# Optimization experiments

Measured on AMD Instinct MI355X. Metric: run time of the kernel, lower is better.

Reference implementation:

```python
import jax, jax.numpy as jnp
import numpy as np

MARGIN = 2.0   # self.m
SCALE = 30.0   # cosine-head logit scale


def setup_inputs() -> dict:
    key = jax.random.key(0)
    k1, k2, k3 = jax.random.split(key, 3)
    B, D, C = 8192, 256, 5994
    emb = jax.random.normal(k1, (B, D), dtype=jnp.float32)
    W = jax.random.normal(k2, (C, D), dtype=jnp.float32) * 0.05
    y = jax.random.randint(k3, (B,), 0, C, dtype=jnp.int32)
    # first half domain 0 (main), second half domain 1 (target)
    y_d = jnp.concatenate([jnp.zeros(B // 2, jnp.int32), jnp.ones(B // 2, jnp.int32)])
    return {"emb": emb, "W": W, "y": y, "y_d": y_d}


def _clf_head(emb, W, y):
    # cosine-similarity classifier + cross-entropy (standard ASV clf head)
    e = emb / (jnp.linalg.norm(emb, axis=1, keepdims=True) + 1e-12)
    w = W / (jnp.linalg.norm(W, axis=1, keepdims=True) + 1e-12)
    logits = SCALE * (e @ w.T)                     # [B, C]
    logp = jax.nn.log_softmax(logits, axis=-1)
    loss = -jnp.mean(jnp.take_along_axis(logp, y[:, None], axis=1))
    acc = jnp.mean((jnp.argmax(logits, axis=-1) == y).astype(jnp.float32))
    return loss, acc


def reference(emb, W, y, y_d):
    B, D = emb.shape
    H = B // 2
    idx = jnp.arange(B)
    # faithful scatter: domain-0 rows -> main_emb[i]; domain-1 rows -> target_emb[i % H]
    # out-of-range sentinel H is dropped (rows with wrong domain stay zero)
    main_idx = jnp.where(y_d == 0, idx, H)
    tgt_idx = jnp.where(y_d != 0, idx % H, H)
    main_emb = jnp.zeros((H, D), emb.dtype).at[main_idx].set(emb, mode="drop")
    target_emb = jnp.zeros((H, D), emb.dtype).at[tgt_idx].set(emb, mode="drop")

    loss_c, acc = _clf_head(emb, W, y)

    # pairwise diffs: even rows main[i]-main[(i+1)%H] (label 1), odd rows main[i]-target[i] (label 0)
    pos_diff = main_emb - jnp.roll(main_emb, -1, axis=0)  # [H, D]
    neg_diff = main_emb - target_emb                      # [H, D]
    das_diff = jnp.stack([pos_diff, neg_diff], axis=1).reshape(B, D)
    das_label = jnp.tile(jnp.array([1.0, 0.0], emb.dtype), H)  # [B]

    das_dist = jnp.linalg.norm(das_diff, axis=1)
    das_loss = jnp.mean((1.0 - das_label) * das_dist ** 2
                        + das_label * jnp.maximum(MARGIN - das_dist, 0.0) ** 2)
    das_dist_mean = jnp.mean(jax.lax.stop_gradient(das_dist))
    return (loss_c, das_loss, acc, das_dist_mean)
```

## Files before the change

### kernel.cpp

```cpp
#include <hip/hip_runtime.h>
#include <hip/hip_bf16.h>

#define B_ROWS 8192
#define DIM 256
#define C_CLS 5994
#define N_CHUNK 188
#define NSPL 16
#define H_HALF 4096
#define SCALE_F 30.0f
#define MAXL 30.0f
#define EXPC 43.2808512266689f

#if defined(__has_builtin)
#if __has_builtin(__builtin_amdgcn_exp2f)
#define EXP2(x) __builtin_amdgcn_exp2f(x)
#endif
#endif
#ifndef EXP2
#define EXP2(x) exp2f(x)
#endif

typedef float f32x16 __attribute__((ext_vector_type(16)));
typedef long long ll;
typedef ll ll2 __attribute__((ext_vector_type(2)));

__global__ __launch_bounds__(256)
void k_pack(const float* __restrict__ emb, const float* __restrict__ W,
            char* __restrict__ en_blk, char* __restrict__ wn_blk,
            float* __restrict__ rne, float* __restrict__ rnw,
            float* __restrict__ accum) {
  __shared__ float ssm[256];
  __shared__ float rnl[32];
  const int b = blockIdx.x;
  const int t = threadIdx.x;
  if (b == 0 && t < 8) accum[t] = 0.f;
  const bool isW = b >= (B_ROWS/32);
  const int tile = isW ? b - (B_ROWS/32) : b;
  const int l31 = t & 31;
  const int row = tile*32 + l31;
  const float* __restrict__ src = isW ? W : emb;
  const bool rv = (!isW) || (row < C_CLS);

  float v[4][8];
  float ss = 0.f;
  #pragma unroll
  for (int i=0;i<4;i++) {
    const int d0 = ((t>>6) + i*4)*16 + ((t>>5)&1)*8;
    if (rv) {
      float4 x0 = *(const float4*)(src + (size_t)row*DIM + d0);
      float4 x1 = *(const float4*)(src + (size_t)row*DIM + d0 + 4);
      v[i][0]=x0.x; v[i][1]=x0.y; v[i][2]=x0.z; v[i][3]=x0.w;
      v[i][4]=x1.x; v[i][5]=x1.y; v[i][6]=x1.z; v[i][7]=x1.w;
      ss += x0.x*x0.x + x0.y*x0.y + x0.z*x0.z + x0.w*x0.w
          + x1.x*x1.x + x1.y*x1.y + x1.z*x1.z + x1.w*x1.w;
    } else {
      #pragma unroll
      for (int j=0;j<8;j++) v[i][j] = 0.f;
    }
  }
  ssm[t] = ss;
  __syncthreads();
  if (t < 32) {
    float s = 0.f;
    #pragma unroll
    for (int j=0;j<8;j++) s += ssm[t + j*32];
    float rn = 1.0f/(sqrtf(s) + 1e-12f);
    rnl[t] = rn;
    int rw = tile*32 + t;
    if (!isW) rne[rw] = rn;
    else if (rw < C_CLS) rnw[rw] = rn;
  }
  __syncthreads();
  const float rn = rnl[l31];
  char* __restrict__ dst = (isW ? wn_blk : en_blk) + (size_t)tile*8192;
  const int kbase = (t>>5)*512 + l31*16;
  (void)kbase;
  #pragma unroll
  for (int i=0;i<4;i++) {
    const int kk = (t>>6) + i*4;
    const int off = (kk>>1)*1024 + ((t>>5)&1)*512 + l31*16 + (kk&1)*8;
    int d0 = 0, d1 = 0;
    d0 = __builtin_amdgcn_cvt_pk_fp8_f32(v[i][0]*rn, v[i][1]*rn, d0, false);
    d0 = __builtin_amdgcn_cvt_pk_fp8_f32(v[i][2]*rn, v[i][3]*rn, d0, true);
    d1 = __builtin_amdgcn_cvt_pk_fp8_f32(v[i][4]*rn, v[i][5]*rn, d1, false);
    d1 = __builtin_amdgcn_cvt_pk_fp8_f32(v[i][6]*rn, v[i][7]*rn, d1, true);
    uint2 u; u.x = (unsigned)d0; u.y = (unsigned)d1;
    *(uint2*)(dst + off) = u;
  }
}

__global__ __launch_bounds__(256, 2)
void k_logits(const char* __restrict__ en_blk, const char* __restrict__ wn_blk,
              float* __restrict__ psum, unsigned* __restrict__ pkey) {
  const int split = blockIdx.x & (NSPL-1);
  const int panel = blockIdx.x / NSPL;
  const int wid  = threadIdx.x >> 6;
  const int lane = threadIdx.x & 63;
  const int l31  = lane & 31;
  const int lh   = lane >> 5;
  const int tile = panel*4 + wid;
  (void)lh;

  ll2 a[8];
  const char* ab = en_blk + (size_t)tile*8192 + lane*16;
  #pragma unroll
  for (int j=0;j<8;j++) a[j] = *(const ll2*)(ab + j*1024);

  float ssum[16]; unsigned key[16];
  #pragma unroll
  for (int r=0;r<16;r++){ ssum[r]=0.f; key[r]=0u; }

  const int nit = (N_CHUNK - split + NSPL - 1) / NSPL;
  const char* p = wn_blk + (size_t)split*8192 + lane*16;
  const ptrdiff_t STEP = (ptrdiff_t)NSPL*8192;

  ll2 b0[4], b1[4];
  #pragma unroll
  for (int j=0;j<4;j++) b0[j] = *(const ll2*)(p + j*1024);
  #pragma unroll
  for (int j=0;j<4;j++) b1[j] = *(const ll2*)(p + (j+4)*1024);

  unsigned colu = (unsigned)(split*32 + l31);
  for (int it = 0; it < nit-1; ++it) {
    const char* pn = p + STEP;
    f32x16 acc = {};
    #pragma unroll
    for (int j=0;j<4;j++) {
      acc = __builtin_amdgcn_mfma_f32_32x32x16_fp8_fp8(a[j][0], b0[j][0], acc, 0,0,0);
      acc = __builtin_amdgcn_mfma_f32_32x32x16_fp8_fp8(a[j][1], b0[j][1], acc, 0,0,0);
    }
    #pragma unroll
    for (int j=0;j<4;j++) b0[j] = *(const ll2*)(pn + j*1024);
    #pragma unroll
    for (int j=0;j<4;j++) {
      acc = __builtin_amdgcn_mfma_f32_32x32x16_fp8_fp8(a[j+4][0], b1[j][0], acc, 0,0,0);
      acc = __builtin_amdgcn_mfma_f32_32x32x16_fp8_fp8(a[j+4][1], b1[j][1], acc, 0,0,0);
    }
    #pragma unroll
    for (int j=0;j<4;j++) b1[j] = *(const ll2*)(pn + (j+4)*1024);
    #pragma unroll
    for (int r=0;r<16;r++) {
      float x = acc[r];
      ssum[r] += EXP2(fmaf(x, EXPC, -EXPC));
      unsigned ky = (__float_as_uint(x + 2.0f) & 0xFFFFE000u) | colu;
      key[r] = ky > key[r] ? ky : key[r];
    }
    colu += NSPL*32;
    p = pn;
  }
  {
    f32x16 acc = {};
    #pragma unroll
    for (int j=0;j<4;j++) {
      acc = __builtin_amdgcn_mfma_f32_32x32x16_fp8_fp8(a[j][0], b0[j][0], acc, 0,0,0);
      acc = __builtin_amdgcn_mfma_f32_32x32x16_fp8_fp8(a[j][1], b0[j][1], acc, 0,0,0);
    }
    #pragma unroll
    for (int j=0;j<4;j++) {
      acc = __builtin_amdgcn_mfma_f32_32x32x16_fp8_fp8(a[j+4][0], b1[j][0], acc, 0,0,0);
      acc = __builtin_amdgcn_mfma_f32_32x32x16_fp8_fp8(a[j+4][1], b1[j][1], acc, 0,0,0);
    }
    #pragma unroll
    for (int r=0;r<16;r++) {
      float x = acc[r];
      ssum[r] += EXP2(fmaf(x, EXPC, -EXPC));
      unsigned ky = (__float_as_uint(x + 2.0f) & 0xFFFFE000u) | colu;
      key[r] = ky > key[r] ? ky : key[r];
    }
  }

  #pragma unroll
  for (int off=1; off<32; off<<=1) {
    #pragma unroll
    for (int r=0;r<16;r++) {
      ssum[r] += __shfl_xor(ssum[r], off);
      unsigned o = __shfl_xor(key[r], off);
      key[r] = o > key[r] ? o : key[r];
    }
  }
  if (l31 == 0) {
    const int rowbase = tile*32;
    #pragma unroll
    for (int r=0;r<16;r++) {
      int row = rowbase + (r&3) + 8*(r>>2) + 4*(lane>>5);
      psum[split*B_ROWS + row] = ssum[r];
      pkey[split*B_ROWS + row] = key[r];
    }
  }
}

__global__ __launch_bounds__(256)
void k_tail(const float* __restrict__ emb, const float* __restrict__ W,
            const int* __restrict__ y, const int* __restrict__ y_d,
            const float* __restrict__ rne, const float* __restrict__ rnw,
            const float* __restrict__ psum, const unsigned* __restrict__ pkey,
            float* __restrict__ accum, float* __restrict__ out) {
  __shared__ float s0[4], s1[4];
  const int wid = threadIdx.x >> 6, lane = threadIdx.x & 63;
  if (blockIdx.x < 128) {
    float lacc = 0.f, cacc = 0.f;
    for (int row = blockIdx.x*4 + wid; row < B_ROWS; row += 512) {
      const int yc = y[row];
      float4 e = *(const float4*)(emb + (size_t)row*DIM + lane*4);
      float4 w = *(const float4*)(W + (size_t)yc*DIM + lane*4);
      float d = e.x*w.x + e.y*w.y + e.z*w.z + e.w*w.w;
      #pragma unroll
      for (int off=1; off<64; off<<=1) d += __shfl_xor(d, off);
      float S = 0.f; unsigned km = 0u;
      if (lane < NSPL) {
        S = psum[lane*B_ROWS + row];
        km = pkey[lane*B_ROWS + row];
      }
      #pragma unroll
      for (int off=1; off<NSPL; off<<=1) {
        S += __shfl_xor(S, off);
        unsigned o = __shfl_xor(km, off);
        if (o > km) km = o;
      }
      if (lane == 0) {
        float ly = SCALE_F * d * rne[row] * rnw[yc];
        lacc += MAXL + logf(S) - ly;
        cacc += ((km & 0x1FFFu) == (unsigned)yc) ? 1.f : 0.f;
      }
    }
    if (lane == 0) { s0[wid] = lacc; s1[wid] = cacc; }
    __syncthreads();
    if (threadIdx.x == 0) {
      atomicAdd(&accum[0], s0[0]+s0[1]+s0[2]+s0[3]);
      atomicAdd(&accum[1], s1[0]+s1[1]+s1[2]+s1[3]);
    }
  } else {
    float a2 = 0.f, a3 = 0.f;
    for (int i = (blockIdx.x-128)*4 + wid; i < H_HALF; i += 256) {
      const int j = (i+1) & (H_HALF-1);
      const int di = y_d[i], dj = y_d[j], dih = y_d[i + H_HALF];
      float4 z = {0.f,0.f,0.f,0.f};
      float4 mi = (di==0)  ? *(const float4*)(emb + (size_t)i*DIM + lane*4) : z;
      float4 mj = (dj==0)  ? *(const float4*)(emb + (size_t)j*DIM + lane*4) : z;
      float4 ti = (dih!=0) ? *(const float4*)(emb + (size_t)(i+H_HALF)*DIM + lane*4)
                           : ((di!=0) ? *(const float4*)(emb + (size_t)i*DIM + lane*4) : z);
      float px = mi.x-mj.x, py = mi.y-mj.y, pz = mi.z-mj.z, pw = mi.w-mj.w;
      float nx = mi.x-ti.x, ny = mi.y-ti.y, nz = mi.z-ti.z, nw = mi.w-ti.w;
      float sp = px*px+py*py+pz*pz+pw*pw;
      float sn = nx*nx+ny*ny+nz*nz+nw*nw;
      #pragma unroll
      for (int off=1; off<64; off<<=1) { sp += __shfl_xor(sp, off); sn += __shfl_xor(sn, off); }
      if (lane == 0) {
        float dp = sqrtf(sp), dn = sqrtf(sn);
        float m = fmaxf(2.0f - dp, 0.f);
        a2 += m*m + dn*dn;
        a3 += dp + dn;
      }
    }
    if (lane == 0) { s0[wid] = a2; s1[wid] = a3; }
    __syncthreads();
    if (threadIdx.x == 0) {
      atomicAdd(&accum[2], s0[0]+s0[1]+s0[2]+s0[3]);
      atomicAdd(&accum[3], s1[0]+s1[1]+s1[2]+s1[3]);
    }
  }
  if (threadIdx.x == 0) {
    __threadfence();
    unsigned* cnt = (unsigned*)(accum + 4);
    unsigned done = atomicAdd(cnt, 1u);
    if (done == 191u) {
      float v0 = atomicAdd(&accum[0], 0.f);
      float v1 = atomicAdd(&accum[1], 0.f);
      float v2 = atomicAdd(&accum[2], 0.f);
      float v3 = atomicAdd(&accum[3], 0.f);
      out[0] = v0 * (1.0f/B_ROWS);
      out[1] = v2 * (1.0f/B_ROWS);
      out[2] = v1 * (1.0f/B_ROWS);
      out[3] = v3 * (1.0f/B_ROWS);
    }
  }
}

extern "C" void kernel_launch(void* const* d_in, const int* in_sizes, int n_in,
                              void* d_out, int out_size, void* d_ws, size_t ws_size,
                              hipStream_t stream) {
  const float* emb = (const float*)d_in[0];
  const float* W   = (const float*)d_in[1];
  const int*   y   = (const int*)d_in[2];
  const int*   y_d = (const int*)d_in[3];

  char* ws = (char*)d_ws;
  const size_t EN_OFF   = 0;
  const size_t WN_OFF   = EN_OFF  + (size_t)256*8192;
  const size_t RNE_OFF  = WN_OFF  + (size_t)N_CHUNK*8192;
  const size_t RNW_OFF  = RNE_OFF + (size_t)B_ROWS*4;
  const size_t PSUM_OFF = RNW_OFF + 24064;
  const size_t PKEY_OFF = PSUM_OFF + (size_t)NSPL*B_ROWS*4;
  const size_t ACC_OFF  = PKEY_OFF + (size_t)NSPL*B_ROWS*4;

  char*     en_blk = ws + EN_OFF;
  char*     wn_blk = ws + WN_OFF;
  float*    rne   = (float*)(ws + RNE_OFF);
  float*    rnw   = (float*)(ws + RNW_OFF);
  float*    psum  = (float*)(ws + PSUM_OFF);
  unsigned* pkey  = (unsigned*)(ws + PKEY_OFF);
  float*    accum = (float*)(ws + ACC_OFF);

  k_pack<<<B_ROWS/32 + N_CHUNK, 256, 0, stream>>>(emb, W, en_blk, wn_blk, rne, rnw, accum);
  k_logits<<<64*NSPL, 256, 0, stream>>>(en_blk, wn_blk, psum, pkey);
  k_tail<<<192, 256, 0, stream>>>(emb, W, y, y_d, rne, rnw, psum, pkey, accum, (float*)d_out);
}
```

Before: 67.47 us.

## Split contrastive-distance work into its own kernel and replace atomics with partial-sum buffers

Moves the domain-pair distance computation out of the tail into a separate k_das kernel launched before the logits kernel, so the tail only handles the classifier merge. The tail now uses 512 blocks, and each block writes its partial sums to its own buffer slot instead of doing float atomicAdds. The last block reduces all partials deterministically. The psum/pkey layout becomes row-major over splits, so the 16 split values for a row are contiguous when the tail reads them. This adds an extra kernel launch in exchange for more tail parallelism and no atomic contention.

```diff
diff --git a/kernel.cpp b/kernel.cpp
--- a/kernel.cpp
+++ b/kernel.cpp
@@ -6,6 +6,9 @@
 #define C_CLS 5994
 #define N_CHUNK 188
 #define NSPL 16
+#define NPACK 444
+#define NDAS 128
+#define NMERGE 512
 #define H_HALF 4096
 #define SCALE_F 30.0f
 #define MAXL 30.0f
@@ -28,12 +31,12 @@
 void k_pack(const float* __restrict__ emb, const float* __restrict__ W,
             char* __restrict__ en_blk, char* __restrict__ wn_blk,
             float* __restrict__ rne, float* __restrict__ rnw,
-            float* __restrict__ accum) {
+            unsigned* __restrict__ cnt) {
   __shared__ float ssm[256];
   __shared__ float rnl[32];
   const int b = blockIdx.x;
   const int t = threadIdx.x;
-  if (b == 0 && t < 8) accum[t] = 0.f;
+  if (b == 0 && t == 0) *cnt = 0u;
   const bool isW = b >= (B_ROWS/32);
   const int tile = isW ? b - (B_ROWS/32) : b;
   const int l31 = t & 31;
@@ -73,8 +76,6 @@
   __syncthreads();
   const float rn = rnl[l31];
   char* __restrict__ dst = (isW ? wn_blk : en_blk) + (size_t)tile*8192;
-  const int kbase = (t>>5)*512 + l31*16;
-  (void)kbase;
   #pragma unroll
   for (int i=0;i<4;i++) {
     const int kk = (t>>6) + i*4;
@@ -89,6 +90,41 @@
   }
 }
 
+__global__ __launch_bounds__(256)
+void k_das(const float* __restrict__ emb, const int* __restrict__ y_d,
+           float* __restrict__ dasL, float* __restrict__ dasD) {
+  __shared__ float s0[4], s1[4];
+  const int wid = threadIdx.x >> 6, lane = threadIdx.x & 63;
+  float a2 = 0.f, a3 = 0.f;
+  for (int i = blockIdx.x*4 + wid; i < H_HALF; i += NDAS*4) {
+    const int j = (i+1) & (H_HALF-1);
+    const int di = y_d[i], dj = y_d[j], dih = y_d[i + H_HALF];
+    float4 z = {0.f,0.f,0.f,0.f};
+    float4 mi = (di==0)  ? *(const float4*)(emb + (size_t)i*DIM + lane*4) : z;
+    float4 mj = (dj==0)  ? *(const float4*)(emb + (size_t)j*DIM + lane*4) : z;
+    float4 ti = (dih!=0) ? *(const float4*)(emb + (size_t)(i+H_HALF)*DIM + lane*4)
+                         : ((di!=0) ? *(const float4*)(emb + (size_t)i*DIM + lane*4) : z);
+    float px = mi.x-mj.x, py = mi.y-mj.y, pz = mi.z-mj.z, pw = mi.w-mj.w;
+    float nx = mi.x-ti.x, ny = mi.y-ti.y, nz = mi.z-ti.z, nw = mi.w-ti.w;
+    float sp = px*px+py*py+pz*pz+pw*pw;
+    float sn = nx*nx+ny*ny+nz*nz+nw*nw;
+    #pragma unroll
+    for (int off=1; off<64; off<<=1) { sp += __shfl_xor(sp, off); sn += __shfl_xor(sn, off); }
+    if (lane == 0) {
+      float dp = sqrtf(sp), dn = sqrtf(sn);
+      float m = fmaxf(2.0f - dp, 0.f);
+      a2 += m*m + dn*dn;
+      a3 += dp + dn;
+    }
+  }
+  if (lane == 0) { s0[wid] = a2; s1[wid] = a3; }
+  __syncthreads();
+  if (threadIdx.x == 0) {
+    dasL[blockIdx.x] = s0[0]+s0[1]+s0[2]+s0[3];
+    dasD[blockIdx.x] = s1[0]+s1[1]+s1[2]+s1[3];
+  }
+}
+
 __global__ __launch_bounds__(256, 2)
 void k_logits(const char* __restrict__ en_blk, const char* __restrict__ wn_blk,
               float* __restrict__ psum, unsigned* __restrict__ pkey) {
@@ -97,9 +133,7 @@
   const int wid  = threadIdx.x >> 6;
   const int lane = threadIdx.x & 63;
   const int l31  = lane & 31;
-  const int lh   = lane >> 5;
   const int tile = panel*4 + wid;
-  (void)lh;
 
   ll2 a[8];
   const char* ab = en_blk + (size_t)tile*8192 + lane*16;
@@ -183,95 +217,77 @@
     #pragma unroll
     for (int r=0;r<16;r++) {
       int row = rowbase + (r&3) + 8*(r>>2) + 4*(lane>>5);
-      psum[split*B_ROWS + row] = ssum[r];
-      pkey[split*B_ROWS + row] = key[r];
+      psum[(size_t)row*NSPL + split] = ssum[r];
+      pkey[(size_t)row*NSPL + split] = key[r];
     }
   }
 }
 
 __global__ __launch_bounds__(256)
 void k_tail(const float* __restrict__ emb, const float* __restrict__ W,
-            const int* __restrict__ y, const int* __restrict__ y_d,
+            const int* __restrict__ y,
             const float* __restrict__ rne, const float* __restrict__ rnw,
             const float* __restrict__ psum, const unsigned* __restrict__ pkey,
-            float* __restrict__ accum, float* __restrict__ out) {
+            float* __restrict__ lossP, float* __restrict__ corrP,
+            const float* __restrict__ dasL, const float* __restrict__ dasD,
+            unsigned* __restrict__ cnt, float* __restrict__ out) {
   __shared__ float s0[4], s1[4];
+  __shared__ int isLast;
   const int wid = threadIdx.x >> 6, lane = threadIdx.x & 63;
-  if (blockIdx.x < 128) {
-    float lacc = 0.f, cacc = 0.f;
-    for (int row = blockIdx.x*4 + wid; row < B_ROWS; row += 512) {
-      const int yc = y[row];
-      float4 e = *(const float4*)(emb + (size_t)row*DIM + lane*4);
-      float4 w = *(const float4*)(W + (size_t)yc*DIM + lane*4);
-      float d = e.x*w.x + e.y*w.y + e.z*w.z + e.w*w.w;
-      #pragma unroll
-      for (int off=1; off<64; off<<=1) d += __shfl_xor(d, off);
-      float S = 0.f; unsigned km = 0u;
-      if (lane < NSPL) {
-        S = psum[lane*B_ROWS + row];
-        km = pkey[lane*B_ROWS + row];
-      }
-      #pragma unroll
-      for (int off=1; off<NSPL; off<<=1) {
-        S += __shfl_xor(S, off);
-        unsigned o = __shfl_xor(km, off);
-        if (o > km) km = o;
-      }
-      if (lane == 0) {
-        float ly = SCALE_F * d * rne[row] * rnw[yc];
-        lacc += MAXL + logf(S) - ly;
-        cacc += ((km & 0x1FFFu) == (unsigned)yc) ? 1.f : 0.f;
-      }
-    }
-    if (lane == 0) { s0[wid] = lacc; s1[wid] = cacc; }
+  float lacc = 0.f, cacc = 0.f;
+  for (int row = blockIdx.x*4 + wid; row < B_ROWS; row += NMERGE*4) {
+    const int yc = y[row];
+    float4 e = *(const float4*)(emb + (size_t)row*DIM + lane*4);
+    float4 w = *(const float4*)(W + (size_t)yc*DIM + lane*4);
+    float d = e.x*w.x + e.y*w.y + e.z*w.z + e.w*w.w;
+    #pragma unroll
+    for (int off=1; off<64; off<<=1) d += __shfl_xor(d, off);
+    float S = 0.f; unsigned km = 0u;
+    if (lane < NSPL) {
+      S = psum[(size_t)row*NSPL + lane];
+      km = pkey[(size_t)row*NSPL + lane];
+    }
+    #pragma unroll
+    for (int off=1; off<NSPL; off<<=1) {
+      S += __shfl_xor(S, off);
+      unsigned o = __shfl_xor(km, off);
+      if (o > km) km = o;
+    }
+    if (lane == 0) {
+      float ly = SCALE_F * d * rne[row] * rnw[yc];
+      lacc += MAXL + logf(S) - ly;
+      cacc += ((km & 0x1FFFu) == (unsigned)yc) ? 1.f : 0.f;
+    }
+  }
+  if (lane == 0) { s0[wid] = lacc; s1[wid] = cacc; }
+  __syncthreads();
+  if (threadIdx.x == 0) {
+    lossP[blockIdx.x] = s0[0]+s0[1]+s0[2]+s0[3];
+    corrP[blockIdx.x] = s1[0]+s1[1]+s1[2]+s1[3];
+    __threadfence();
+    unsigned done = atomicAdd(cnt, 1u);
+    isLast = (done == NMERGE-1u) ? 1 : 0;
+  }
+  __syncthreads();
+  if (isLast) {
+    const int t = threadIdx.x;
+    float lv = atomicAdd(&lossP[t], 0.f) + atomicAdd(&lossP[t+256], 0.f);
+    float cv = atomicAdd(&corrP[t], 0.f) + atomicAdd(&corrP[t+256], 0.f);
+    float dl = (t < NDAS) ? atomicAdd((float*)&dasL[t], 0.f) : 0.f;
+    float dd = (t < NDAS) ? atomicAdd((float*)&dasD[t], 0.f) : 0.f;
+    #pragma unroll
+    for (int off=1; off<64; off<<=1) {
+      lv += __shfl_xor(lv, off); cv += __shfl_xor(cv, off);
+      dl += __shfl_xor(dl, off); dd += __shfl_xor(dd, off);
+    }
+    __shared__ float r4[4][4];
+    if (lane == 0) { r4[wid][0]=lv; r4[wid][1]=cv; r4[wid][2]=dl; r4[wid][3]=dd; }
     __syncthreads();
-    if (threadIdx.x == 0) {
-      atomicAdd(&accum[0], s0[0]+s0[1]+s0[2]+s0[3]);
-      atomicAdd(&accum[1], s1[0]+s1[1]+s1[2]+s1[3]);
-    }
-  } else {
-    float a2 = 0.f, a3 = 0.f;
-    for (int i = (blockIdx.x-128)*4 + wid; i < H_HALF; i += 256) {
-      const int j = (i+1) & (H_HALF-1);
-      const int di = y_d[i], dj = y_d[j], dih = y_d[i + H_HALF];
-      float4 z = {0.f,0.f,0.f,0.f};
-      float4 mi = (di==0)  ? *(const float4*)(emb + (size_t)i*DIM + lane*4) : z;
-      float4 mj = (dj==0)  ? *(const float4*)(emb + (size_t)j*DIM + lane*4) : z;
-      float4 ti = (dih!=0) ? *(const float4*)(emb + (size_t)(i+H_HALF)*DIM + lane*4)
-                           : ((di!=0) ? *(const float4*)(emb + (size_t)i*DIM + lane*4) : z);
-      float px = mi.x-mj.x, py = mi.y-mj.y, pz = mi.z-mj.z, pw = mi.w-mj.w;
-      float nx = mi.x-ti.x, ny = mi.y-ti.y, nz = mi.z-ti.z, nw = mi.w-ti.w;
-      float sp = px*px+py*py+pz*pz+pw*pw;
-      float sn = nx*nx+ny*ny+nz*nz+nw*nw;
-      #pragma unroll
-      for (int off=1; off<64; off<<=1) { sp += __shfl_xor(sp, off); sn += __shfl_xor(sn, off); }
-      if (lane == 0) {
-        float dp = sqrtf(sp), dn = sqrtf(sn);
-        float m = fmaxf(2.0f - dp, 0.f);
-        a2 += m*m + dn*dn;
-        a3 += dp + dn;
-      }
-    }
-    if (lane == 0) { s0[wid] = a2; s1[wid] = a3; }
-    __syncthreads();
-    if (threadIdx.x == 0) {
-      atomicAdd(&accum[2], s0[0]+s0[1]+s0[2]+s0[3]);
-      atomicAdd(&accum[3], s1[0]+s1[1]+s1[2]+s1[3]);
-    }
-  }
-  if (threadIdx.x == 0) {
-    __threadfence();
-    unsigned* cnt = (unsigned*)(accum + 4);
-    unsigned done = atomicAdd(cnt, 1u);
-    if (done == 191u) {
-      float v0 = atomicAdd(&accum[0], 0.f);
-      float v1 = atomicAdd(&accum[1], 0.f);
-      float v2 = atomicAdd(&accum[2], 0.f);
-      float v3 = atomicAdd(&accum[3], 0.f);
-      out[0] = v0 * (1.0f/B_ROWS);
-      out[1] = v2 * (1.0f/B_ROWS);
-      out[2] = v1 * (1.0f/B_ROWS);
-      out[3] = v3 * (1.0f/B_ROWS);
+    if (t == 0) {
+      out[0] = (r4[0][0]+r4[1][0]+r4[2][0]+r4[3][0]) * (1.0f/B_ROWS);
+      out[1] = (r4[0][2]+r4[1][2]+r4[2][2]+r4[3][2]) * (1.0f/B_ROWS);
+      out[2] = (r4[0][1]+r4[1][1]+r4[2][1]+r4[3][1]) * (1.0f/B_ROWS);
+      out[3] = (r4[0][3]+r4[1][3]+r4[2][3]+r4[3][3]) * (1.0f/B_ROWS);
     }
   }
 }
@@ -291,7 +307,11 @@
   const size_t RNW_OFF  = RNE_OFF + (size_t)B_ROWS*4;
   const size_t PSUM_OFF = RNW_OFF + 24064;
   const size_t PKEY_OFF = PSUM_OFF + (size_t)NSPL*B_ROWS*4;
-  const size_t ACC_OFF  = PKEY_OFF + (size_t)NSPL*B_ROWS*4;
+  const size_t LP_OFF   = PKEY_OFF + (size_t)NSPL*B_ROWS*4;
+  const size_t CP_OFF   = LP_OFF   + NMERGE*4;
+  const size_t DL_OFF   = CP_OFF   + NMERGE*4;
+  const size_t DD_OFF   = DL_OFF   + NDAS*4;
+  const size_t CNT_OFF  = DD_OFF   + NDAS*4;
 
   char*     en_blk = ws + EN_OFF;
   char*     wn_blk = ws + WN_OFF;
@@ -299,9 +319,15 @@
   float*    rnw   = (float*)(ws + RNW_OFF);
   float*    psum  = (float*)(ws + PSUM_OFF);
   unsigned* pkey  = (unsigned*)(ws + PKEY_OFF);
-  float*    accum = (float*)(ws + ACC_OFF);
-
-  k_pack<<<B_ROWS/32 + N_CHUNK, 256, 0, stream>>>(emb, W, en_blk, wn_blk, rne, rnw, accum);
+  float*    lossP = (float*)(ws + LP_OFF);
+  float*    corrP = (float*)(ws + CP_OFF);
+  float*    dasL  = (float*)(ws + DL_OFF);
+  float*    dasD  = (float*)(ws + DD_OFF);
+  unsigned* cnt   = (unsigned*)(ws + CNT_OFF);
+
+  k_pack<<<NPACK, 256, 0, stream>>>(emb, W, en_blk, wn_blk, rne, rnw, cnt);
+  k_das<<<NDAS, 256, 0, stream>>>(emb, y_d, dasL, dasD);
   k_logits<<<64*NSPL, 256, 0, stream>>>(en_blk, wn_blk, psum, pkey);
-  k_tail<<<192, 256, 0, stream>>>(emb, W, y, y_d, rne, rnw, psum, pkey, accum, (float*)d_out);
-}
+  k_tail<<<NMERGE, 256, 0, stream>>>(emb, W, y, rne, rnw, psum, pkey,
+                                     lossP, corrP, dasL, dasD, cnt, (float*)d_out);
+}
```

Result: slower. 71.14 us (+5.4%).

## Double-buffer MFMA accumulators, halve column splits, recompute norms in tail

Applied to the files above, without the earlier changes.

The logits loop now alternates between two accumulators, so the exp/argmax epilogue of one chunk overlaps the MFMAs of the next. Column splits drop from 16 to 8, which halves the grid and the partial-sum traffic but gives each block a longer serial loop. The pack kernel no longer writes per-row inverse norms. The tail recomputes the emb and W norms with extra shuffle reductions, trading more tail arithmetic for less workspace traffic.

```diff
diff --git a/kernel.cpp b/kernel.cpp
--- a/kernel.cpp
+++ b/kernel.cpp
@@ -5,7 +5,8 @@
 #define DIM 256
 #define C_CLS 5994
 #define N_CHUNK 188
-#define NSPL 16
+#define NSPL 8
+#define NPACK 444
 #define H_HALF 4096
 #define SCALE_F 30.0f
 #define MAXL 30.0f
@@ -27,7 +28,6 @@
 __global__ __launch_bounds__(256)
 void k_pack(const float* __restrict__ emb, const float* __restrict__ W,
             char* __restrict__ en_blk, char* __restrict__ wn_blk,
-            float* __restrict__ rne, float* __restrict__ rnw,
             float* __restrict__ accum) {
   __shared__ float ssm[256];
   __shared__ float rnl[32];
@@ -64,17 +64,11 @@
     float s = 0.f;
     #pragma unroll
     for (int j=0;j<8;j++) s += ssm[t + j*32];
-    float rn = 1.0f/(sqrtf(s) + 1e-12f);
-    rnl[t] = rn;
-    int rw = tile*32 + t;
-    if (!isW) rne[rw] = rn;
-    else if (rw < C_CLS) rnw[rw] = rn;
+    rnl[t] = 1.0f/(sqrtf(s) + 1e-12f);
   }
   __syncthreads();
   const float rn = rnl[l31];
   char* __restrict__ dst = (isW ? wn_blk : en_blk) + (size_t)tile*8192;
-  const int kbase = (t>>5)*512 + l31*16;
-  (void)kbase;
   #pragma unroll
   for (int i=0;i<4;i++) {
     const int kk = (t>>6) + i*4;
@@ -97,9 +91,7 @@
   const int wid  = threadIdx.x >> 6;
   const int lane = threadIdx.x & 63;
   const int l31  = lane & 31;
-  const int lh   = lane >> 5;
   const int tile = panel*4 + wid;
-  (void)lh;
 
   ll2 a[8];
   const char* ab = en_blk + (size_t)tile*8192 + lane*16;
@@ -120,54 +112,56 @@
   #pragma unroll
   for (int j=0;j<4;j++) b1[j] = *(const ll2*)(p + (j+4)*1024);
 
-  unsigned colu = (unsigned)(split*32 + l31);
-  for (int it = 0; it < nit-1; ++it) {
-    const char* pn = p + STEP;
-    f32x16 acc = {};
-    #pragma unroll
-    for (int j=0;j<4;j++) {
-      acc = __builtin_amdgcn_mfma_f32_32x32x16_fp8_fp8(a[j][0], b0[j][0], acc, 0,0,0);
-      acc = __builtin_amdgcn_mfma_f32_32x32x16_fp8_fp8(a[j][1], b0[j][1], acc, 0,0,0);
-    }
-    #pragma unroll
-    for (int j=0;j<4;j++) b0[j] = *(const ll2*)(pn + j*1024);
-    #pragma unroll
-    for (int j=0;j<4;j++) {
-      acc = __builtin_amdgcn_mfma_f32_32x32x16_fp8_fp8(a[j+4][0], b1[j][0], acc, 0,0,0);
-      acc = __builtin_amdgcn_mfma_f32_32x32x16_fp8_fp8(a[j+4][1], b1[j][1], acc, 0,0,0);
-    }
-    #pragma unroll
-    for (int j=0;j<4;j++) b1[j] = *(const ll2*)(pn + (j+4)*1024);
-    #pragma unroll
-    for (int r=0;r<16;r++) {
-      float x = acc[r];
-      ssum[r] += EXP2(fmaf(x, EXPC, -EXPC));
-      unsigned ky = (__float_as_uint(x + 2.0f) & 0xFFFFE000u) | colu;
-      key[r] = ky > key[r] ? ky : key[r];
-    }
-    colu += NSPL*32;
-    p = pn;
-  }
-  {
-    f32x16 acc = {};
-    #pragma unroll
-    for (int j=0;j<4;j++) {
-      acc = __builtin_amdgcn_mfma_f32_32x32x16_fp8_fp8(a[j][0], b0[j][0], acc, 0,0,0);
-      acc = __builtin_amdgcn_mfma_f32_32x32x16_fp8_fp8(a[j][1], b0[j][1], acc, 0,0,0);
-    }
-    #pragma unroll
-    for (int j=0;j<4;j++) {
-      acc = __builtin_amdgcn_mfma_f32_32x32x16_fp8_fp8(a[j+4][0], b1[j][0], acc, 0,0,0);
-      acc = __builtin_amdgcn_mfma_f32_32x32x16_fp8_fp8(a[j+4][1], b1[j][1], acc, 0,0,0);
-    }
-    #pragma unroll
-    for (int r=0;r<16;r++) {
-      float x = acc[r];
-      ssum[r] += EXP2(fmaf(x, EXPC, -EXPC));
-      unsigned ky = (__float_as_uint(x + 2.0f) & 0xFFFFE000u) | colu;
-      key[r] = ky > key[r] ? ky : key[r];
-    }
-  }
+  int c = split;
+  f32x16 accA = {}, accB = {};
+  unsigned cluA = 0, cluB = 0;
+
+#define MFMA_CHUNK(ACC) do { \
+    const char* pn_ = p + STEP; \
+    const bool pf_ = (c + NSPL) < N_CHUNK; \
+    _Pragma("unroll") \
+    for (int j=0;j<4;j++) { \
+      ACC = __builtin_amdgcn_mfma_f32_32x32x16_fp8_fp8(a[j][0], b0[j][0], ACC, 0,0,0); \
+      ACC = __builtin_amdgcn_mfma_f32_32x32x16_fp8_fp8(a[j][1], b0[j][1], ACC, 0,0,0); \
+    } \
+    if (pf_) { _Pragma("unroll") for (int j=0;j<4;j++) b0[j] = *(const ll2*)(pn_ + j*1024); } \
+    _Pragma("unroll") \
+    for (int j=0;j<4;j++) { \
+      ACC = __builtin_amdgcn_mfma_f32_32x32x16_fp8_fp8(a[j+4][0], b1[j][0], ACC, 0,0,0); \
+      ACC = __builtin_amdgcn_mfma_f32_32x32x16_fp8_fp8(a[j+4][1], b1[j][1], ACC, 0,0,0); \
+    } \
+    if (pf_) { _Pragma("unroll") for (int j=0;j<4;j++) b1[j] = *(const ll2*)(pn_ + (j+4)*1024); } \
+    p = pn_; c += NSPL; \
+  } while (0)
+
+#define EPI(ACC, CLU) do { \
+    _Pragma("unroll") \
+    for (int r=0;r<16;r++) { \
+      float x_ = ACC[r];                         \
+      ssum[r] += EXP2(fmaf(x_, EXPC, -EXPC)); \
+      unsigned ky_ = (__float_as_uint(x_ + 2.0f) & 0xFFFFE000u) | (CLU); \
+      key[r] = ky_ > key[r] ? ky_ : key[r]; \
+    } \
+  } while (0)
+
+  cluA = (unsigned)(c*32 + l31);
+  MFMA_CHUNK(accA);
+  for (int it = 1; it < nit; ++it) {
+    if (it & 1) {
+      cluB = (unsigned)(c*32 + l31);
+      MFMA_CHUNK(accB);
+      EPI(accA, cluA);
+      accA = (f32x16){};
+    } else {
+      cluA = (unsigned)(c*32 + l31);
+      MFMA_CHUNK(accA);
+      EPI(accB, cluB);
+      accB = (f32x16){};
+    }
+  }
+  if ((nit - 1) & 1) EPI(accB, cluB); else EPI(accA, cluA);
+#undef MFMA_CHUNK
+#undef EPI
 
   #pragma unroll
   for (int off=1; off<32; off<<=1) {
@@ -192,7 +186,6 @@
 __global__ __launch_bounds__(256)
 void k_tail(const float* __restrict__ emb, const float* __restrict__ W,
             const int* __restrict__ y, const int* __restrict__ y_d,
-            const float* __restrict__ rne, const float* __restrict__ rnw,
             const float* __restrict__ psum, const unsigned* __restrict__ pkey,
             float* __restrict__ accum, float* __restrict__ out) {
   __shared__ float s0[4], s1[4];
@@ -204,8 +197,12 @@
       float4 e = *(const float4*)(emb + (size_t)row*DIM + lane*4);
       float4 w = *(const float4*)(W + (size_t)yc*DIM + lane*4);
       float d = e.x*w.x + e.y*w.y + e.z*w.z + e.w*w.w;
+      float e2 = e.x*e.x + e.y*e.y + e.z*e.z + e.w*e.w;
+      float w2 = w.x*w.x + w.y*w.y + w.z*w.z + w.w*w.w;
       #pragma unroll
-      for (int off=1; off<64; off<<=1) d += __shfl_xor(d, off);
+      for (int off=1; off<64; off<<=1) {
+        d += __shfl_xor(d, off); e2 += __shfl_xor(e2, off); w2 += __shfl_xor(w2, off);
+      }
       float S = 0.f; unsigned km = 0u;
       if (lane < NSPL) {
         S = psum[lane*B_ROWS + row];
@@ -218,7 +215,7 @@
         if (o > km) km = o;
       }
       if (lane == 0) {
-        float ly = SCALE_F * d * rne[row] * rnw[yc];
+        float ly = SCALE_F * d / ((sqrtf(e2) + 1e-12f) * (sqrtf(w2) + 1e-12f));
         lacc += MAXL + logf(S) - ly;
         cacc += ((km & 0x1FFFu) == (unsigned)yc) ? 1.f : 0.f;
       }
@@ -287,21 +284,17 @@
   char* ws = (char*)d_ws;
   const size_t EN_OFF   = 0;
   const size_t WN_OFF   = EN_OFF  + (size_t)256*8192;
-  const size_t RNE_OFF  = WN_OFF  + (size_t)N_CHUNK*8192;
-  const size_t RNW_OFF  = RNE_OFF + (size_t)B_ROWS*4;
-  const size_t PSUM_OFF = RNW_OFF + 24064;
+  const size_t PSUM_OFF = WN_OFF  + (size_t)N_CHUNK*8192;
   const size_t PKEY_OFF = PSUM_OFF + (size_t)NSPL*B_ROWS*4;
   const size_t ACC_OFF  = PKEY_OFF + (size_t)NSPL*B_ROWS*4;
 
   char*     en_blk = ws + EN_OFF;
   char*     wn_blk = ws + WN_OFF;
-  float*    rne   = (float*)(ws + RNE_OFF);
-  float*    rnw   = (float*)(ws + RNW_OFF);
   float*    psum  = (float*)(ws + PSUM_OFF);
   unsigned* pkey  = (unsigned*)(ws + PKEY_OFF);
   float*    accum = (float*)(ws + ACC_OFF);
 
-  k_pack<<<B_ROWS/32 + N_CHUNK, 256, 0, stream>>>(emb, W, en_blk, wn_blk, rne, rnw, accum);
+  k_pack<<<NPACK, 256, 0, stream>>>(emb, W, en_blk, wn_blk, accum);
   k_logits<<<64*NSPL, 256, 0, stream>>>(en_blk, wn_blk, psum, pkey);
-  k_tail<<<192, 256, 0, stream>>>(emb, W, y, y_d, rne, rnw, psum, pkey, accum, (float*)d_out);
+  k_tail<<<192, 256, 0, stream>>>(emb, W, y, y_d, psum, pkey, accum, (float*)d_out);
 }
```

New measurement: 67.53 us. Within noise of the previous version (+0.1%).

## Rebalance GEMM splits, co-schedule DAS work with logits, recompute norms in tail

Applied to the files above, without the earlier changes.

Halves the column split count so each logits block does twice the chunks with fewer partials to merge. The DAS distance computation moves from the tail kernel into the logits launch as extra blocks so it runs alongside the GEMM. The MFMA chain is split into two independent accumulators to shorten the dependency chain. The tail now recomputes row norms itself instead of reading stored reciprocal norms, and uses more blocks. Fewer splits mean fewer blocks in the GEMM grid (512), which may lower occupancy across CUs.

```diff
diff --git a/kernel.cpp b/kernel.cpp
--- a/kernel.cpp
+++ b/kernel.cpp
@@ -5,7 +5,11 @@
 #define DIM 256
 #define C_CLS 5994
 #define N_CHUNK 188
-#define NSPL 16
+#define NSPL 8
+#define NPACK 444
+#define NGEMM 512
+#define NDAS 64
+#define NMERGE 384
 #define H_HALF 4096
 #define SCALE_F 30.0f
 #define MAXL 30.0f
@@ -27,7 +31,6 @@
 __global__ __launch_bounds__(256)
 void k_pack(const float* __restrict__ emb, const float* __restrict__ W,
             char* __restrict__ en_blk, char* __restrict__ wn_blk,
-            float* __restrict__ rne, float* __restrict__ rnw,
             float* __restrict__ accum) {
   __shared__ float ssm[256];
   __shared__ float rnl[32];
@@ -64,17 +67,11 @@
     float s = 0.f;
     #pragma unroll
     for (int j=0;j<8;j++) s += ssm[t + j*32];
-    float rn = 1.0f/(sqrtf(s) + 1e-12f);
-    rnl[t] = rn;
-    int rw = tile*32 + t;
-    if (!isW) rne[rw] = rn;
-    else if (rw < C_CLS) rnw[rw] = rn;
+    rnl[t] = 1.0f/(sqrtf(s) + 1e-12f);
   }
   __syncthreads();
   const float rn = rnl[l31];
   char* __restrict__ dst = (isW ? wn_blk : en_blk) + (size_t)tile*8192;
-  const int kbase = (t>>5)*512 + l31*16;
-  (void)kbase;
   #pragma unroll
   for (int i=0;i<4;i++) {
     const int kk = (t>>6) + i*4;
@@ -91,147 +88,18 @@
 
 __global__ __launch_bounds__(256, 2)
 void k_logits(const char* __restrict__ en_blk, const char* __restrict__ wn_blk,
-              float* __restrict__ psum, unsigned* __restrict__ pkey) {
-  const int split = blockIdx.x & (NSPL-1);
-  const int panel = blockIdx.x / NSPL;
+              const float* __restrict__ emb, const int* __restrict__ y_d,
+              float* __restrict__ psum, unsigned* __restrict__ pkey,
+              float* __restrict__ accum) {
+  const int b = blockIdx.x;
   const int wid  = threadIdx.x >> 6;
   const int lane = threadIdx.x & 63;
-  const int l31  = lane & 31;
-  const int lh   = lane >> 5;
-  const int tile = panel*4 + wid;
-  (void)lh;
-
-  ll2 a[8];
-  const char* ab = en_blk + (size_t)tile*8192 + lane*16;
-  #pragma unroll
-  for (int j=0;j<8;j++) a[j] = *(const ll2*)(ab + j*1024);
-
-  float ssum[16]; unsigned key[16];
-  #pragma unroll
-  for (int r=0;r<16;r++){ ssum[r]=0.f; key[r]=0u; }
-
-  const int nit = (N_CHUNK - split + NSPL - 1) / NSPL;
-  const char* p = wn_blk + (size_t)split*8192 + lane*16;
-  const ptrdiff_t STEP = (ptrdiff_t)NSPL*8192;
-
-  ll2 b0[4], b1[4];
-  #pragma unroll
-  for (int j=0;j<4;j++) b0[j] = *(const ll2*)(p + j*1024);
-  #pragma unroll
-  for (int j=0;j<4;j++) b1[j] = *(const ll2*)(p + (j+4)*1024);
-
-  unsigned colu = (unsigned)(split*32 + l31);
-  for (int it = 0; it < nit-1; ++it) {
-    const char* pn = p + STEP;
-    f32x16 acc = {};
-    #pragma unroll
-    for (int j=0;j<4;j++) {
-      acc = __builtin_amdgcn_mfma_f32_32x32x16_fp8_fp8(a[j][0], b0[j][0], acc, 0,0,0);
-      acc = __builtin_amdgcn_mfma_f32_32x32x16_fp8_fp8(a[j][1], b0[j][1], acc, 0,0,0);
-    }
-    #pragma unroll
-    for (int j=0;j<4;j++) b0[j] = *(const ll2*)(pn + j*1024);
-    #pragma unroll
-    for (int j=0;j<4;j++) {
-      acc = __builtin_amdgcn_mfma_f32_32x32x16_fp8_fp8(a[j+4][0], b1[j][0], acc, 0,0,0);
-      acc = __builtin_amdgcn_mfma_f32_32x32x16_fp8_fp8(a[j+4][1], b1[j][1], acc, 0,0,0);
-    }
-    #pragma unroll
-    for (int j=0;j<4;j++) b1[j] = *(const ll2*)(pn + (j+4)*1024);
-    #pragma unroll
-    for (int r=0;r<16;r++) {
-      float x = acc[r];
-      ssum[r] += EXP2(fmaf(x, EXPC, -EXPC));
-      unsigned ky = (__float_as_uint(x + 2.0f) & 0xFFFFE000u) | colu;
-      key[r] = ky > key[r] ? ky : key[r];
-    }
-    colu += NSPL*32;
-    p = pn;
-  }
-  {
-    f32x16 acc = {};
-    #pragma unroll
-    for (int j=0;j<4;j++) {
-      acc = __builtin_amdgcn_mfma_f32_32x32x16_fp8_fp8(a[j][0], b0[j][0], acc, 0,0,0);
-      acc = __builtin_amdgcn_mfma_f32_32x32x16_fp8_fp8(a[j][1], b0[j][1], acc, 0,0,0);
-    }
-    #pragma unroll
-    for (int j=0;j<4;j++) {
-      acc = __builtin_amdgcn_mfma_f32_32x32x16_fp8_fp8(a[j+4][0], b1[j][0], acc, 0,0,0);
-      acc = __builtin_amdgcn_mfma_f32_32x32x16_fp8_fp8(a[j+4][1], b1[j][1], acc, 0,0,0);
-    }
-    #pragma unroll
-    for (int r=0;r<16;r++) {
-      float x = acc[r];
-      ssum[r] += EXP2(fmaf(x, EXPC, -EXPC));
-      unsigned ky = (__float_as_uint(x + 2.0f) & 0xFFFFE000u) | colu;
-      key[r] = ky > key[r] ? ky : key[r];
-    }
-  }
-
-  #pragma unroll
-  for (int off=1; off<32; off<<=1) {
-    #pragma unroll
-    for (int r=0;r<16;r++) {
-      ssum[r] += __shfl_xor(ssum[r], off);
-      unsigned o = __shfl_xor(key[r], off);
-      key[r] = o > key[r] ? o : key[r];
-    }
-  }
-  if (l31 == 0) {
-    const int rowbase = tile*32;
-    #pragma unroll
-    for (int r=0;r<16;r++) {
-      int row = rowbase + (r&3) + 8*(r>>2) + 4*(lane>>5);
-      psum[split*B_ROWS + row] = ssum[r];
-      pkey[split*B_ROWS + row] = key[r];
-    }
-  }
-}
-
-__global__ __launch_bounds__(256)
-void k_tail(const float* __restrict__ emb, const float* __restrict__ W,
-            const int* __restrict__ y, const int* __restrict__ y_d,
-            const float* __restrict__ rne, const float* __restrict__ rnw,
-            const float* __restrict__ psum, const unsigned* __restrict__ pkey,
-            float* __restrict__ accum, float* __restrict__ out) {
-  __shared__ float s0[4], s1[4];
-  const int wid = threadIdx.x >> 6, lane = threadIdx.x & 63;
-  if (blockIdx.x < 128) {
-    float lacc = 0.f, cacc = 0.f;
-    for (int row = blockIdx.x*4 + wid; row < B_ROWS; row += 512) {
-      const int yc = y[row];
-      float4 e = *(const float4*)(emb + (size_t)row*DIM + lane*4);
-      float4 w = *(const float4*)(W + (size_t)yc*DIM + lane*4);
-      float d = e.x*w.x + e.y*w.y + e.z*w.z + e.w*w.w;
-      #pragma unroll
-      for (int off=1; off<64; off<<=1) d += __shfl_xor(d, off);
-      float S = 0.f; unsigned km = 0u;
-      if (lane < NSPL) {
-        S = psum[lane*B_ROWS + row];
-        km = pkey[lane*B_ROWS + row];
-      }
-      #pragma unroll
-      for (int off=1; off<NSPL; off<<=1) {
-        S += __shfl_xor(S, off);
-        unsigned o = __shfl_xor(km, off);
-        if (o > km) km = o;
-      }
-      if (lane == 0) {
-        float ly = SCALE_F * d * rne[row] * rnw[yc];
-        lacc += MAXL + logf(S) - ly;
-        cacc += ((km & 0x1FFFu) == (unsigned)yc) ? 1.f : 0.f;
-      }
-    }
-    if (lane == 0) { s0[wid] = lacc; s1[wid] = cacc; }
-    __syncthreads();
-    if (threadIdx.x == 0) {
-      atomicAdd(&accum[0], s0[0]+s0[1]+s0[2]+s0[3]);
-      atomicAdd(&accum[1], s1[0]+s1[1]+s1[2]+s1[3]);
-    }
-  } else {
+
+  if (b >= NGEMM) {
+    __shared__ float s0[4], s1[4];
+    const int bd = b - NGEMM;
     float a2 = 0.f, a3 = 0.f;
-    for (int i = (blockIdx.x-128)*4 + wid; i < H_HALF; i += 256) {
+    for (int i = bd*4 + wid; i < H_HALF; i += NDAS*4) {
       const int j = (i+1) & (H_HALF-1);
       const int di = y_d[i], dj = y_d[j], dih = y_d[i + H_HALF];
       float4 z = {0.f,0.f,0.f,0.f};
@@ -258,12 +126,143 @@
       atomicAdd(&accum[2], s0[0]+s0[1]+s0[2]+s0[3]);
       atomicAdd(&accum[3], s1[0]+s1[1]+s1[2]+s1[3]);
     }
+    return;
+  }
+
+  const int split = b & (NSPL-1);
+  const int panel = b / NSPL;
+  const int l31  = lane & 31;
+  const int tile = panel*4 + wid;
+
+  ll2 a[8];
+  const char* ab = en_blk + (size_t)tile*8192 + lane*16;
+  #pragma unroll
+  for (int j=0;j<8;j++) a[j] = *(const ll2*)(ab + j*1024);
+
+  float ssum[16]; unsigned key[16];
+  #pragma unroll
+  for (int r=0;r<16;r++){ ssum[r]=0.f; key[r]=0u; }
+
+  const int nit = (N_CHUNK - split + NSPL - 1) / NSPL;
+  const char* p = wn_blk + (size_t)split*8192 + lane*16;
+  const ptrdiff_t STEP = (ptrdiff_t)NSPL*8192;
+
+  ll2 b0[4], b1[4];
+  #pragma unroll
+  for (int j=0;j<4;j++) b0[j] = *(const ll2*)(p + j*1024);
+  #pragma unroll
+  for (int j=0;j<4;j++) b1[j] = *(const ll2*)(p + (j+4)*1024);
+
+  unsigned colu = (unsigned)(split*32 + l31);
+  for (int it = 0; it < nit-1; ++it) {
+    const char* pn = p + STEP;
+    f32x16 acc0 = {}, acc1 = {};
+    #pragma unroll
+    for (int j=0;j<4;j++) {
+      acc0 = __builtin_amdgcn_mfma_f32_32x32x16_fp8_fp8(a[j][0],   b0[j][0], acc0, 0,0,0);
+      acc1 = __builtin_amdgcn_mfma_f32_32x32x16_fp8_fp8(a[j+4][0], b1[j][0], acc1, 0,0,0);
+      acc0 = __builtin_amdgcn_mfma_f32_32x32x16_fp8_fp8(a[j][1],   b0[j][1], acc0, 0,0,0);
+      acc1 = __builtin_amdgcn_mfma_f32_32x32x16_fp8_fp8(a[j+4][1], b1[j][1], acc1, 0,0,0);
+    }
+    #pragma unroll
+    for (int j=0;j<4;j++) b0[j] = *(const ll2*)(pn + j*1024);
+    #pragma unroll
+    for (int j=0;j<4;j++) b1[j] = *(const ll2*)(pn + (j+4)*1024);
+    #pragma unroll
+    for (int r=0;r<16;r++) {
+      float x = acc0[r] + acc1[r];
+      ssum[r] += EXP2(fmaf(x, EXPC, -EXPC));
+      unsigned ky = (__float_as_uint(x + 2.0f) & 0xFFFFE000u) | colu;
+      key[r] = ky > key[r] ? ky : key[r];
+    }
+    colu += NSPL*32;
+    p = pn;
+  }
+  {
+    f32x16 acc0 = {}, acc1 = {};
+    #pragma unroll
+    for (int j=0;j<4;j++) {
+      acc0 = __builtin_amdgcn_mfma_f32_32x32x16_fp8_fp8(a[j][0],   b0[j][0], acc0, 0,0,0);
+      acc1 = __builtin_amdgcn_mfma_f32_32x32x16_fp8_fp8(a[j+4][0], b1[j][0], acc1, 0,0,0);
+      acc0 = __builtin_amdgcn_mfma_f32_32x32x16_fp8_fp8(a[j][1],   b0[j][1], acc0, 0,0,0);
+      acc1 = __builtin_amdgcn_mfma_f32_32x32x16_fp8_fp8(a[j+4][1], b1[j][1], acc1, 0,0,0);
+    }
+    #pragma unroll
+    for (int r=0;r<16;r++) {
+      float x = acc0[r] + acc1[r];
+      ssum[r] += EXP2(fmaf(x, EXPC, -EXPC));
+      unsigned ky = (__float_as_uint(x + 2.0f) & 0xFFFFE000u) | colu;
+      key[r] = ky > key[r] ? ky : key[r];
+    }
+  }
+
+  #pragma unroll
+  for (int off=1; off<32; off<<=1) {
+    #pragma unroll
+    for (int r=0;r<16;r++) {
+      ssum[r] += __shfl_xor(ssum[r], off);
+      unsigned o = __shfl_xor(key[r], off);
+      key[r] = o > key[r] ? o : key[r];
+    }
+  }
+  if (l31 == 0) {
+    const int rowbase = tile*32;
+    #pragma unroll
+    for (int r=0;r<16;r++) {
+      int row = rowbase + (r&3) + 8*(r>>2) + 4*(lane>>5);
+      psum[split*B_ROWS + row] = ssum[r];
+      pkey[split*B_ROWS + row] = key[r];
+    }
+  }
+}
+
+__global__ __launch_bounds__(256)
+void k_tail(const float* __restrict__ emb, const float* __restrict__ W,
+            const int* __restrict__ y,
+            const float* __restrict__ psum, const unsigned* __restrict__ pkey,
+            float* __restrict__ accum, float* __restrict__ out) {
+  __shared__ float s0[4], s1[4];
+  const int wid = threadIdx.x >> 6, lane = threadIdx.x & 63;
+  float lacc = 0.f, cacc = 0.f;
+  for (int row = blockIdx.x*4 + wid; row < B_ROWS; row += NMERGE*4) {
+    const int yc = y[row];
+    float4 e = *(const float4*)(emb + (size_t)row*DIM + lane*4);
+    float4 w = *(const float4*)(W + (size_t)yc*DIM + lane*4);
+    float d = e.x*w.x + e.y*w.y + e.z*w.z + e.w*w.w;
+    float e2 = e.x*e.x + e.y*e.y + e.z*e.z + e.w*e.w;
+    float w2 = w.x*w.x + w.y*w.y + w.z*w.z + w.w*w.w;
+    #pragma unroll
+    for (int off=1; off<64; off<<=1) {
+      d += __shfl_xor(d, off); e2 += __shfl_xor(e2, off); w2 += __shfl_xor(w2, off);
+    }
+    float S = 0.f; unsigned km = 0u;
+    if (lane < NSPL) {
+      S = psum[lane*B_ROWS + row];
+      km = pkey[lane*B_ROWS + row];
+    }
+    #pragma unroll
+    for (int off=1; off<NSPL; off<<=1) {
+      S += __shfl_xor(S, off);
+      unsigned o = __shfl_xor(km, off);
+      if (o > km) km = o;
+    }
+    if (lane == 0) {
+      float ly = SCALE_F * d / ((sqrtf(e2) + 1e-12f) * (sqrtf(w2) + 1e-12f));
+      lacc += MAXL + logf(S) - ly;
+      cacc += ((km & 0x1FFFu) == (unsigned)yc) ? 1.f : 0.f;
+    }
+  }
+  if (lane == 0) { s0[wid] = lacc; s1[wid] = cacc; }
+  __syncthreads();
+  if (threadIdx.x == 0) {
+    atomicAdd(&accum[0], s0[0]+s0[1]+s0[2]+s0[3]);
+    atomicAdd(&accum[1], s1[0]+s1[1]+s1[2]+s1[3]);
   }
   if (threadIdx.x == 0) {
     __threadfence();
     unsigned* cnt = (unsigned*)(accum + 4);
     unsigned done = atomicAdd(cnt, 1u);
-    if (done == 191u) {
+    if (done == NMERGE-1u) {
       float v0 = atomicAdd(&accum[0], 0.f);
       float v1 = atomicAdd(&accum[1], 0.f);
       float v2 = atomicAdd(&accum[2], 0.f);
@@ -287,21 +286,17 @@
   char* ws = (char*)d_ws;
   const size_t EN_OFF   = 0;
   const size_t WN_OFF   = EN_OFF  + (size_t)256*8192;
-  const size_t RNE_OFF  = WN_OFF  + (size_t)N_CHUNK*8192;
-  const size_t RNW_OFF  = RNE_OFF + (size_t)B_ROWS*4;
-  const size_t PSUM_OFF = RNW_OFF + 24064;
+  const size_t PSUM_OFF = WN_OFF  + (size_t)N_CHUNK*8192;
   const size_t PKEY_OFF = PSUM_OFF + (size_t)NSPL*B_ROWS*4;
   const size_t ACC_OFF  = PKEY_OFF + (size_t)NSPL*B_ROWS*4;
 
   char*     en_blk = ws + EN_OFF;
   char*     wn_blk = ws + WN_OFF;
-  float*    rne   = (float*)(ws + RNE_OFF);
-  float*    rnw   = (float*)(ws + RNW_OFF);
   float*    psum  = (float*)(ws + PSUM_OFF);
   unsigned* pkey  = (unsigned*)(ws + PKEY_OFF);
   float*    accum = (float*)(ws + ACC_OFF);
 
-  k_pack<<<B_ROWS/32 + N_CHUNK, 256, 0, stream>>>(emb, W, en_blk, wn_blk, rne, rnw, accum);
-  k_logits<<<64*NSPL, 256, 0, stream>>>(en_blk, wn_blk, psum, pkey);
-  k_tail<<<192, 256, 0, stream>>>(emb, W, y, y_d, rne, rnw, psum, pkey, accum, (float*)d_out);
+  k_pack<<<NPACK, 256, 0, stream>>>(emb, W, en_blk, wn_blk, accum);
+  k_logits<<<NGEMM + NDAS, 256, 0, stream>>>(en_blk, wn_blk, emb, y_d, psum, pkey, accum);
+  k_tail<<<NMERGE, 256, 0, stream>>>(emb, W, y, psum, pkey, accum, (float*)d_out);
 }
```

Measured after the change: 73.32 us. +8.7%, slower.
